# Kernel tuning notes

Hardware: AMD Instinct MI355X
Metric: run time of the kernel (lower is better)

## Reference

```python
import jax, jax.numpy as jnp
import numpy as np

N_NODES = 50000
N_EDGES = 1600000
D_FEAT = 32
SCALE = 1.0
EPS = 1e-12


def setup_inputs() -> dict:
    key = jax.random.key(0)
    k1, k2 = jax.random.split(key)
    x = jax.random.normal(k1, (N_NODES, D_FEAT), dtype=jnp.float32)
    edge_index = jax.random.randint(k2, (2, N_EDGES), 0, N_NODES, dtype=jnp.int32)
    return {"x": x, "edge_index": edge_index}


def reference(x, edge_index):
    index_i = edge_index[0]  # target nodes (segments)
    index_j = edge_index[1]  # source nodes (gathered)

    # in-degree per target node, clamped to 1 (torch_scatter 'mean' semantics:
    # empty segments get mean 0)
    ones = jnp.ones((index_i.shape[0],), dtype=x.dtype)
    deg = jax.ops.segment_sum(ones, index_i, num_segments=N_NODES)
    deg = jnp.maximum(deg, 1.0)[:, None]  # [N, 1]

    # neighborhood mean of features
    mean = jax.ops.segment_sum(x[index_j], index_i, num_segments=N_NODES) / deg

    # neighborhood mean of squared deviations -> std
    reduced_x = (x - mean) ** 2
    var = jax.ops.segment_sum(reduced_x[index_j], index_i, num_segments=N_NODES) / deg
    std = jnp.sqrt(var + EPS)

    out = SCALE * x / std
    # replace infs with the original x, as in the torch module
    out = jnp.where(jnp.isinf(out), x, out)
    return out
```

## Files before the change

kernel.cpp:

```cpp
#include <hip/hip_runtime.h>
#include <hip/hip_fp16.h>
#include <math.h>

#define DF 32
#define EPSF 1e-12f
#define PB 128
#define PB_SHIFT 7
#define NBMAX 512
#define CAP 5120
#define CHUNK 4096
#define EPT 16

__global__ __launch_bounds__(256) void k_passA(
    const int* __restrict__ ii, const int* __restrict__ jj,
    const float* __restrict__ x, int* __restrict__ gcount,
    unsigned int* __restrict__ bucketed, __half* __restrict__ xh,
    int ne, int nb, int nfeat) {
  __shared__ int hist[NBMAX];
  __shared__ int histc[NBMAX];
  __shared__ int bb[NBMAX];
  __shared__ int excl_s[NBMAX];
  __shared__ int sc[256];
  __shared__ unsigned int stage[CHUNK];
  int t = threadIdx.x;
  hist[t] = 0; hist[t + 256] = 0;
  __syncthreads();

  int base = blockIdx.x * CHUNK;
  unsigned int pk[EPT];
  int rk[EPT];
#pragma unroll
  for (int k = 0; k < EPT; ++k) {
    int e = base + t + k * 256;
    if (e < ne) {
      int i = ii[e], j = jj[e];
      int b = i >> PB_SHIFT;
      pk[k] = ((unsigned)b << 23) | ((unsigned)(i & (PB - 1)) << 16) | (unsigned)j;
      rk[k] = atomicAdd(&hist[b], 1);
    } else {
      rk[k] = -1;
    }
  }

  {
    int base8 = blockIdx.x * (CHUNK / 8);
#pragma unroll
    for (int r = 0; r < 2; ++r) {
      int p8 = base8 + r * 256 + t;
      if (p8 * 8 < nfeat) {
        float4 a = ((const float4*)x)[2 * p8];
        float4 bq = ((const float4*)x)[2 * p8 + 1];
        union { __half2 h[4]; float4 f; } u;
        u.h[0] = __floats2half2_rn(a.x, a.y);
        u.h[1] = __floats2half2_rn(a.z, a.w);
        u.h[2] = __floats2half2_rn(bq.x, bq.y);
        u.h[3] = __floats2half2_rn(bq.z, bq.w);
        ((float4*)xh)[p8] = u.f;
      }
    }
  }
  __syncthreads();
  histc[t] = hist[t]; histc[t + 256] = hist[t + 256];
  __syncthreads();
#pragma unroll
  for (int b = t; b < NBMAX; b += 256) {
    int c = histc[b];
    bb[b] = (b < nb && c > 0) ? atomicAdd(&gcount[b], c) : 0;
  }
  int a0 = histc[2 * t], a1 = histc[2 * t + 1];
  sc[t] = a0 + a1;
  __syncthreads();
  int pv = sc[t];
  for (int s = 1; s < 256; s <<= 1) {
    int v = 0;
    if (t >= s) v = sc[t - s];
    __syncthreads();
    if (t >= s) sc[t] += v;
    __syncthreads();
  }
  int eP = sc[t] - pv;
  excl_s[2 * t] = eP;
  excl_s[2 * t + 1] = eP + a0;
  __syncthreads();
#pragma unroll
  for (int k = 0; k < EPT; ++k) {
    if (rk[k] >= 0) {
      int b = pk[k] >> 23;
      stage[excl_s[b] + rk[k]] = pk[k];
    }
  }
  __syncthreads();
  int bcnt = ne - base;
  if (bcnt > CHUNK) bcnt = CHUNK;
  for (int p = t; p < bcnt; p += 256) {
    unsigned int v = stage[p];
    int b = v >> 23;
    int excl = excl_s[b];
    bucketed[(size_t)b * CAP + bb[b] + (p - excl)] = v;
  }
}

__global__ __launch_bounds__(256) void k_sortmean(
    const unsigned int* __restrict__ bucketed, const int* __restrict__ gcount,
    const __half* __restrict__ xh, const float* __restrict__ x,
    __half* __restrict__ yh, unsigned short* __restrict__ sortedj,
    int* __restrict__ deg_g, int* __restrict__ curend_g, int* __restrict__ perm,
    int n_nodes, int nb) {
  __shared__ int sc[256];
  __shared__ int lh[PB];
  __shared__ int lcur[PB];
  __shared__ int dh[PB];
  __shared__ int dcur[PB];
  __shared__ int nstart[PB];
  __shared__ int ndeg[PB];
  __shared__ int npl[PB];
  __shared__ unsigned short sjl[CAP];
  __shared__ int sgbase;
  int b = blockIdx.x, t = threadIdx.x;

  int g0 = (2 * t < nb) ? gcount[2 * t] : 0;
  int g1 = (2 * t + 1 < nb) ? gcount[2 * t + 1] : 0;
  sc[t] = g0 + g1;
  __syncthreads();
  int pv = sc[t];
  for (int s = 1; s < 256; s <<= 1) {
    int v = 0;
    if (t >= s) v = sc[t - s];
    __syncthreads();
    if (t >= s) sc[t] += v;
    __syncthreads();
  }
  if (2 * t == b) sgbase = sc[t] - pv;
  if (2 * t + 1 == b) sgbase = sc[t] - pv + g0;
  if (t < PB) { lh[t] = 0; dh[t] = 0; }
  __syncthreads();
  int gbase = sgbase;
  int cnt = gcount[b];
  const unsigned int* src = bucketed + (size_t)b * CAP;

  for (int p = t; p < cnt; p += 256) atomicAdd(&lh[(src[p] >> 16) & (PB - 1)], 1);
  __syncthreads();
  int a = (t < PB) ? lh[t] : 0;
  if (t < PB) sc[t] = a;
  __syncthreads();
  for (int s = 1; s < PB; s <<= 1) {
    int v = 0;
    if (t < PB && t >= s) v = sc[t - s];
    __syncthreads();
    if (t < PB && t >= s) sc[t] += v;
    __syncthreads();
  }
  int excl = (t < PB) ? sc[t] - a : 0;
  int node = b * PB + t;
  bool nvalid = (t < PB) && (node < n_nodes);
  if (t < PB) { lcur[t] = excl; nstart[t] = excl; ndeg[t] = a; }
  if (nvalid) {
    deg_g[node] = a;
    curend_g[node] = gbase + excl + a;
    atomicAdd(&dh[a < PB - 1 ? a : PB - 1], 1);
  }
  __syncthreads();
  int d0 = (t < PB) ? dh[t] : 0;
  if (t < PB) sc[t] = d0;
  __syncthreads();
  for (int s = 1; s < PB; s <<= 1) {
    int v = 0;
    if (t < PB && t >= s) v = sc[t - s];
    __syncthreads();
    if (t < PB && t >= s) sc[t] += v;
    __syncthreads();
  }
  if (t < PB) dcur[t] = sc[t] - d0;
  __syncthreads();
  if (nvalid) {
    int bin = a < PB - 1 ? a : PB - 1;
    int pos = atomicAdd(&dcur[bin], 1);
    npl[pos] = t;
    perm[b * PB + pos] = node;
  } else if (t < PB) {
    npl[t] = -1;
    perm[b * PB + t] = -1;
  }
  __syncthreads();
  for (int p = t; p < cnt; p += 256) {
    unsigned int v = src[p];
    int il = (v >> 16) & (PB - 1);
    int pos = atomicAdd(&lcur[il], 1);
    sjl[pos] = (unsigned short)(v & 0xFFFFu);
  }
  __syncthreads();
  for (int p = t; p < cnt; p += 256) sortedj[gbase + p] = sjl[p];

  int wvl = t >> 6, lane = t & 63;
  int g = lane >> 3, r = (lane >> 2) & 1, c = lane & 3;
  int co = c * 8;
#pragma unroll
  for (int sweep = 0; sweep < PB / 32; ++sweep) {
    int slot = sweep * 32 + wvl * 8 + g;
    int il = npl[slot];
    bool valid = (il >= 0);
    int dg = valid ? ndeg[il] : 0;
    int st = valid ? nstart[il] : 0;
    int en = st + dg;
    __half2 aA0 = {}, aA1 = {}, aA2 = {}, aA3 = {};
    __half2 aB0 = {}, aB1 = {}, aB2 = {}, aB3 = {};
    int s = st + r;
    for (; s + 6 < en; s += 8) {
      int j0 = sjl[s], j1 = sjl[s + 2], j2 = sjl[s + 4], j3 = sjl[s + 6];
      float4 v0 = *(const float4*)&xh[j0 * DF + co];
      float4 v1 = *(const float4*)&xh[j1 * DF + co];
      float4 v2 = *(const float4*)&xh[j2 * DF + co];
      float4 v3 = *(const float4*)&xh[j3 * DF + co];
      const __half2* h0 = (const __half2*)&v0;
      const __half2* h1 = (const __half2*)&v1;
      const __half2* h2 = (const __half2*)&v2;
      const __half2* h3 = (const __half2*)&v3;
      aA0 = __hadd2(aA0, h0[0]); aA1 = __hadd2(aA1, h0[1]);
      aA2 = __hadd2(aA2, h0[2]); aA3 = __hadd2(aA3, h0[3]);
      aB0 = __hadd2(aB0, h1[0]); aB1 = __hadd2(aB1, h1[1]);
      aB2 = __hadd2(aB2, h1[2]); aB3 = __hadd2(aB3, h1[3]);
      aA0 = __hadd2(aA0, h2[0]); aA1 = __hadd2(aA1, h2[1]);
      aA2 = __hadd2(aA2, h2[2]); aA3 = __hadd2(aA3, h2[3]);
      aB0 = __hadd2(aB0, h3[0]); aB1 = __hadd2(aB1, h3[1]);
      aB2 = __hadd2(aB2, h3[2]); aB3 = __hadd2(aB3, h3[3]);
    }
    for (; s < en; s += 2) {
      int j = sjl[s];
      float4 v = *(const float4*)&xh[j * DF + co];
      const __half2* h = (const __half2*)&v;
      aA0 = __hadd2(aA0, h[0]); aA1 = __hadd2(aA1, h[1]);
      aA2 = __hadd2(aA2, h[2]); aA3 = __hadd2(aA3, h[3]);
    }
    __half2 s0 = __hadd2(aA0, aB0), s1 = __hadd2(aA1, aB1);
    __half2 s2 = __hadd2(aA2, aB2), s3 = __hadd2(aA3, aB3);
    union { __half2 h; int i; } u0, u1, u2, u3;
    u0.h = s0; u1.h = s1; u2.h = s2; u3.h = s3;
    u0.i = __shfl_xor(u0.i, 4); s0 = __hadd2(s0, u0.h);
    u1.i = __shfl_xor(u1.i, 4); s1 = __hadd2(s1, u1.h);
    u2.i = __shfl_xor(u2.i, 4); s2 = __hadd2(s2, u2.h);
    u3.i = __shfl_xor(u3.i, 4); s3 = __hadd2(s3, u3.h);
    if (valid && r == 0) {
      int w = b * PB + il;
      float inv = 1.0f / fmaxf((float)dg, 1.0f);
      float2 m0 = __half22float2(s0);
      float2 m1 = __half22float2(s1);
      float2 m2 = __half22float2(s2);
      float2 m3 = __half22float2(s3);
      float4 xa = *(const float4*)&x[w * DF + co];
      float4 xb = *(const float4*)&x[w * DF + co + 4];
      float d0 = xa.x - m0.x * inv;
      float d1 = xa.y - m0.y * inv;
      float d2 = xa.z - m1.x * inv;
      float d3 = xa.w - m1.y * inv;
      float d4 = xb.x - m2.x * inv;
      float d5 = xb.y - m2.y * inv;
      float d6 = xb.z - m3.x * inv;
      float d7 = xb.w - m3.y * inv;
      union { __half2 h[4]; float4 f; } uo;
      uo.h[0] = __floats2half2_rn(d0 * d0, d1 * d1);
      uo.h[1] = __floats2half2_rn(d2 * d2, d3 * d3);
      uo.h[2] = __floats2half2_rn(d4 * d4, d5 * d5);
      uo.h[3] = __floats2half2_rn(d6 * d6, d7 * d7);
      *(float4*)&yh[w * DF + co] = uo.f;
    }
  }
}

__global__ __launch_bounds__(256) void k_varfinal(
    const int* __restrict__ perm, const unsigned short* __restrict__ sortedj,
    const int* __restrict__ curend, const int* __restrict__ deg,
    const __half* __restrict__ yh, const float* __restrict__ x,
    float* __restrict__ out, int nperm) {
  int wv = (int)((blockIdx.x * blockDim.x + threadIdx.x) >> 6);
  int lane = threadIdx.x & 63;
  int g = lane >> 3;
  int r = (lane >> 2) & 1;
  int c = lane & 3;
  int ni = wv * 8 + g;
  int w = perm[ni];
  bool valid = (w >= 0);
  int dg = valid ? deg[w] : 0;
  int end = valid ? curend[w] : 0;
  int start = end - dg;
  int co = c * 8;
  float accA[8], accB[8];
#pragma unroll
  for (int k = 0; k < 8; ++k) { accA[k] = 0.f; accB[k] = 0.f; }
  int s = start + r;
  for (; s + 6 < end; s += 8) {
    int j0 = sortedj[s], j1 = sortedj[s + 2], j2 = sortedj[s + 4], j3 = sortedj[s + 6];
    float4 v0 = *(const float4*)&yh[j0 * DF + co];
    float4 v1 = *(const float4*)&yh[j1 * DF + co];
    float4 v2 = *(const float4*)&yh[j2 * DF + co];
    float4 v3 = *(const float4*)&yh[j3 * DF + co];
    const __half2* h0 = (const __half2*)&v0;
    const __half2* h1 = (const __half2*)&v1;
    const __half2* h2 = (const __half2*)&v2;
    const __half2* h3 = (const __half2*)&v3;
#pragma unroll
    for (int k = 0; k < 4; ++k) {
      float2 f0 = __half22float2(h0[k]);
      float2 f1 = __half22float2(h1[k]);
      float2 f2 = __half22float2(h2[k]);
      float2 f3 = __half22float2(h3[k]);
      accA[2 * k]     += f0.x + f2.x;
      accA[2 * k + 1] += f0.y + f2.y;
      accB[2 * k]     += f1.x + f3.x;
      accB[2 * k + 1] += f1.y + f3.y;
    }
  }
  for (; s < end; s += 2) {
    int j = sortedj[s];
    float4 v = *(const float4*)&yh[j * DF + co];
    const __half2* h = (const __half2*)&v;
#pragma unroll
    for (int k = 0; k < 4; ++k) {
      float2 f = __half22float2(h[k]);
      accA[2 * k]     += f.x;
      accA[2 * k + 1] += f.y;
    }
  }
  float acc[8];
#pragma unroll
  for (int k = 0; k < 8; ++k) {
    acc[k] = accA[k] + accB[k];
    acc[k] += __shfl_xor(acc[k], 4);
  }
  if (valid && r == 0) {
    float dgc = fmaxf((float)dg, 1.0f);
    float4 xa = *(const float4*)&x[w * DF + co];
    float4 xb = *(const float4*)&x[w * DF + co + 4];
    float xs[8] = {xa.x, xa.y, xa.z, xa.w, xb.x, xb.y, xb.z, xb.w};
    float o[8];
#pragma unroll
    for (int k = 0; k < 8; ++k) {
      float sq = sqrtf(acc[k] / dgc + EPSF);
      o[k] = xs[k] / sq;
      if (isinf(o[k])) o[k] = xs[k];
    }
    float4 oa = {o[0], o[1], o[2], o[3]};
    float4 ob = {o[4], o[5], o[6], o[7]};
    *(float4*)&out[w * DF + co] = oa;
    *(float4*)&out[w * DF + co + 4] = ob;
  }
}

extern "C" void kernel_launch(void* const* d_in, const int* in_sizes, int n_in,
                              void* d_out, int out_size, void* d_ws, size_t ws_size,
                              hipStream_t stream) {
  const float* x = (const float*)d_in[0];
  const int* ei = (const int*)d_in[1];
  const int n_nodes = in_sizes[0] / DF;
  const int ne = in_sizes[1] / 2;
  const int* ii = ei;
  const int* jj = ei + ne;
  const int nb = (n_nodes + PB - 1) / PB;
  const int nfeat = n_nodes * DF;
  const int nperm = nb * PB;

  char* wsb = (char*)d_ws;
  size_t off = 0;
  auto align16 = [](size_t v) { return (v + 15) & ~(size_t)15; };
  int* gcount = (int*)(wsb + off); off = align16(off + NBMAX * 4);
  int* deg    = (int*)(wsb + off); off = align16(off + (size_t)n_nodes * 4);
  int* curend = (int*)(wsb + off); off = align16(off + (size_t)n_nodes * 4);
  int* perm   = (int*)(wsb + off); off = align16(off + (size_t)nperm * 4);
  unsigned short* sortedj = (unsigned short*)(wsb + off);
  off = align16(off + (size_t)ne * 2);
  unsigned int* bucketed = (unsigned int*)(wsb + off);
  off = align16(off + (size_t)nb * CAP * 4);
  __half* xh = (__half*)(wsb + off); off = align16(off + (size_t)nfeat * 2);
  __half* yh = (__half*)(wsb + off);

  float* out = (float*)d_out;

  hipMemsetAsync(gcount, 0, NBMAX * sizeof(int), stream);

  int nblkA = (ne + CHUNK - 1) / CHUNK;
  int nblkF = (nfeat + CHUNK - 1) / CHUNK;
  if (nblkF > nblkA) nblkA = nblkF;
  k_passA<<<nblkA, 256, 0, stream>>>(ii, jj, x, gcount, bucketed, xh, ne, nb, nfeat);
  k_sortmean<<<nb, 256, 0, stream>>>(bucketed, gcount, xh, x, yh, sortedj,
                                     deg, curend, perm, n_nodes, nb);

  int gblocks = nperm / 32;
  k_varfinal<<<gblocks, 256, 0, stream>>>(perm, sortedj, curend, deg, yh, x, out, nperm);
}
```

Measured before the change: 75.72 us.

## Halve bucket size and allocate bucket output offsets with an atomic cursor

Shrinks the node bucket from 128 to 64 nodes and the edge chunk from 4096 to 2048, with the packed-key bit layout, shared histograms and bucket capacity adjusted to match. This roughly doubles the block count of both the bucketing and sort/mean kernels, aiming at better occupancy across the CUs. Each sort/mean block now reserves its output range in sortedj with one global atomicAdd instead of redundantly prefix-scanning all bucket counts, which removes a block-wide scan. As a result, bucket segments are no longer laid out in bucket order, and the smaller capacity leaves less headroom for skewed degree distributions.

Result: slower. 133.5 us (+76.4%).

```diff
diff --git a/kernel.cpp b/kernel.cpp
--- a/kernel.cpp
+++ b/kernel.cpp
@@ -4,12 +4,12 @@
 
 #define DF 32
 #define EPSF 1e-12f
-#define PB 128
-#define PB_SHIFT 7
-#define NBMAX 512
-#define CAP 5120
-#define CHUNK 4096
-#define EPT 16
+#define PB 64
+#define PB_SHIFT 6
+#define NBMAX 1024
+#define CAP 2600
+#define CHUNK 2048
+#define EPT 8
 
 __global__ __launch_bounds__(256) void k_passA(
     const int* __restrict__ ii, const int* __restrict__ jj,
@@ -17,13 +17,13 @@
     unsigned int* __restrict__ bucketed, __half* __restrict__ xh,
     int ne, int nb, int nfeat) {
   __shared__ int hist[NBMAX];
-  __shared__ int histc[NBMAX];
   __shared__ int bb[NBMAX];
   __shared__ int excl_s[NBMAX];
   __shared__ int sc[256];
   __shared__ unsigned int stage[CHUNK];
   int t = threadIdx.x;
-  hist[t] = 0; hist[t + 256] = 0;
+#pragma unroll
+  for (int b4 = t; b4 < NBMAX; b4 += 256) hist[b4] = 0;
   __syncthreads();
 
   int base = blockIdx.x * CHUNK;
@@ -35,7 +35,7 @@
     if (e < ne) {
       int i = ii[e], j = jj[e];
       int b = i >> PB_SHIFT;
-      pk[k] = ((unsigned)b << 23) | ((unsigned)(i & (PB - 1)) << 16) | (unsigned)j;
+      pk[k] = ((unsigned)b << 22) | ((unsigned)(i & (PB - 1)) << 16) | (unsigned)j;
       rk[k] = atomicAdd(&hist[b], 1);
     } else {
       rk[k] = -1;
@@ -43,34 +43,30 @@
   }
 
   {
-    int base8 = blockIdx.x * (CHUNK / 8);
-#pragma unroll
-    for (int r = 0; r < 2; ++r) {
-      int p8 = base8 + r * 256 + t;
-      if (p8 * 8 < nfeat) {
-        float4 a = ((const float4*)x)[2 * p8];
-        float4 bq = ((const float4*)x)[2 * p8 + 1];
-        union { __half2 h[4]; float4 f; } u;
-        u.h[0] = __floats2half2_rn(a.x, a.y);
-        u.h[1] = __floats2half2_rn(a.z, a.w);
-        u.h[2] = __floats2half2_rn(bq.x, bq.y);
-        u.h[3] = __floats2half2_rn(bq.z, bq.w);
-        ((float4*)xh)[p8] = u.f;
-      }
-    }
-  }
-  __syncthreads();
-  histc[t] = hist[t]; histc[t + 256] = hist[t + 256];
-  __syncthreads();
-#pragma unroll
-  for (int b = t; b < NBMAX; b += 256) {
-    int c = histc[b];
-    bb[b] = (b < nb && c > 0) ? atomicAdd(&gcount[b], c) : 0;
-  }
-  int a0 = histc[2 * t], a1 = histc[2 * t + 1];
-  sc[t] = a0 + a1;
-  __syncthreads();
-  int pv = sc[t];
+    int p8 = blockIdx.x * (CHUNK / 8) + t;
+    if (p8 * 8 < nfeat) {
+      float4 a = ((const float4*)x)[2 * p8];
+      float4 bq = ((const float4*)x)[2 * p8 + 1];
+      union { __half2 h[4]; float4 f; } u;
+      u.h[0] = __floats2half2_rn(a.x, a.y);
+      u.h[1] = __floats2half2_rn(a.z, a.w);
+      u.h[2] = __floats2half2_rn(bq.x, bq.y);
+      u.h[3] = __floats2half2_rn(bq.z, bq.w);
+      ((float4*)xh)[p8] = u.f;
+    }
+  }
+  __syncthreads();
+  int h0 = hist[4 * t], h1 = hist[4 * t + 1], h2 = hist[4 * t + 2], h3 = hist[4 * t + 3];
+  {
+    int b0 = 4 * t;
+    bb[b0]     = (b0 < nb && h0 > 0)     ? atomicAdd(&gcount[b0], h0)     : 0;
+    bb[b0 + 1] = (b0 + 1 < nb && h1 > 0) ? atomicAdd(&gcount[b0 + 1], h1) : 0;
+    bb[b0 + 2] = (b0 + 2 < nb && h2 > 0) ? atomicAdd(&gcount[b0 + 2], h2) : 0;
+    bb[b0 + 3] = (b0 + 3 < nb && h3 > 0) ? atomicAdd(&gcount[b0 + 3], h3) : 0;
+  }
+  int s4 = h0 + h1 + h2 + h3;
+  sc[t] = s4;
+  __syncthreads();
   for (int s = 1; s < 256; s <<= 1) {
     int v = 0;
     if (t >= s) v = sc[t - s];
@@ -78,14 +74,16 @@
     if (t >= s) sc[t] += v;
     __syncthreads();
   }
-  int eP = sc[t] - pv;
-  excl_s[2 * t] = eP;
-  excl_s[2 * t + 1] = eP + a0;
+  int gb = sc[t] - s4;
+  excl_s[4 * t] = gb;
+  excl_s[4 * t + 1] = gb + h0;
+  excl_s[4 * t + 2] = gb + h0 + h1;
+  excl_s[4 * t + 3] = gb + h0 + h1 + h2;
   __syncthreads();
 #pragma unroll
   for (int k = 0; k < EPT; ++k) {
     if (rk[k] >= 0) {
-      int b = pk[k] >> 23;
+      int b = pk[k] >> 22;
       stage[excl_s[b] + rk[k]] = pk[k];
     }
   }
@@ -94,14 +92,14 @@
   if (bcnt > CHUNK) bcnt = CHUNK;
   for (int p = t; p < bcnt; p += 256) {
     unsigned int v = stage[p];
-    int b = v >> 23;
-    int excl = excl_s[b];
-    bucketed[(size_t)b * CAP + bb[b] + (p - excl)] = v;
+    int b = v >> 22;
+    bucketed[(size_t)b * CAP + bb[b] + (p - excl_s[b])] = v;
   }
 }
 
 __global__ __launch_bounds__(256) void k_sortmean(
     const unsigned int* __restrict__ bucketed, const int* __restrict__ gcount,
+    int* __restrict__ cursor,
     const __half* __restrict__ xh, const float* __restrict__ x,
     __half* __restrict__ yh, unsigned short* __restrict__ sortedj,
     int* __restrict__ deg_g, int* __restrict__ curend_g, int* __restrict__ perm,
@@ -117,25 +115,12 @@
   __shared__ unsigned short sjl[CAP];
   __shared__ int sgbase;
   int b = blockIdx.x, t = threadIdx.x;
-
-  int g0 = (2 * t < nb) ? gcount[2 * t] : 0;
-  int g1 = (2 * t + 1 < nb) ? gcount[2 * t + 1] : 0;
-  sc[t] = g0 + g1;
-  __syncthreads();
-  int pv = sc[t];
-  for (int s = 1; s < 256; s <<= 1) {
-    int v = 0;
-    if (t >= s) v = sc[t - s];
-    __syncthreads();
-    if (t >= s) sc[t] += v;
-    __syncthreads();
-  }
-  if (2 * t == b) sgbase = sc[t] - pv;
-  if (2 * t + 1 == b) sgbase = sc[t] - pv + g0;
+  int cnt = gcount[b];
+
+  if (t == 0) sgbase = atomicAdd(cursor, cnt);
   if (t < PB) { lh[t] = 0; dh[t] = 0; }
   __syncthreads();
   int gbase = sgbase;
-  int cnt = gcount[b];
   const unsigned int* src = bucketed + (size_t)b * CAP;
 
   for (int p = t; p < cnt; p += 256) atomicAdd(&lh[(src[p] >> 16) & (PB - 1)], 1);
@@ -181,7 +166,6 @@
     npl[t] = -1;
     perm[b * PB + t] = -1;
   }
-  __syncthreads();
   for (int p = t; p < cnt; p += 256) {
     unsigned int v = src[p];
     int il = (v >> 16) & (PB - 1);
@@ -362,6 +346,7 @@
   size_t off = 0;
   auto align16 = [](size_t v) { return (v + 15) & ~(size_t)15; };
   int* gcount = (int*)(wsb + off); off = align16(off + NBMAX * 4);
+  int* cursor = (int*)(wsb + off); off = align16(off + 16);
   int* deg    = (int*)(wsb + off); off = align16(off + (size_t)n_nodes * 4);
   int* curend = (int*)(wsb + off); off = align16(off + (size_t)n_nodes * 4);
   int* perm   = (int*)(wsb + off); off = align16(off + (size_t)nperm * 4);
@@ -374,13 +359,13 @@
 
   float* out = (float*)d_out;
 
-  hipMemsetAsync(gcount, 0, NBMAX * sizeof(int), stream);
+  hipMemsetAsync(gcount, 0, NBMAX * 4 + 16, stream);
 
   int nblkA = (ne + CHUNK - 1) / CHUNK;
   int nblkF = (nfeat + CHUNK - 1) / CHUNK;
   if (nblkF > nblkA) nblkA = nblkF;
   k_passA<<<nblkA, 256, 0, stream>>>(ii, jj, x, gcount, bucketed, xh, ne, nb, nfeat);
-  k_sortmean<<<nb, 256, 0, stream>>>(bucketed, gcount, xh, x, yh, sortedj,
+  k_sortmean<<<nb, 256, 0, stream>>>(bucketed, gcount, cursor, xh, x, yh, sortedj,
                                      deg, curend, perm, n_nodes, nb);
 
   int gblocks = nperm / 32;
```
